# Performance work log

Measured on AMD Instinct MI355X. Metric: run time of the kernel, lower is better.

## Reference

```python
import jax, jax.numpy as jnp
import numpy as np

EPS = 1e-06


def setup_inputs() -> dict:
    key = jax.random.key(0)
    k1, k2 = jax.random.split(key)
    B, S, D = 8, 4096, 1024
    embeddings = jax.random.normal(k1, (B, S, D), dtype=jnp.float32)
    curvature = jax.random.normal(k2, (B, S, D), dtype=jnp.float32)
    gamma = jnp.ones((D,), dtype=jnp.float32)
    beta = jnp.zeros((D,), dtype=jnp.float32)
    curvature_scale = jnp.full((1,), 0.1, dtype=jnp.float32)
    return {
        "embeddings": embeddings,
        "curvature": curvature,
        "gamma": gamma,
        "beta": beta,
        "curvature_scale": curvature_scale,
    }


def reference(embeddings, curvature, gamma, beta, curvature_scale):
    # Field-aware normalization (FieldNormalization.call):
    # standard mean/var norm over features, scaled by local curvature magnitude.
    mean = jnp.mean(embeddings, axis=-1, keepdims=True)          # [B,S,1]
    var = jnp.var(embeddings, axis=-1, keepdims=True)            # [B,S,1]
    normalized = (embeddings - mean) / jnp.sqrt(var + EPS)       # [B,S,D]
    # curvature magnitude per token: sqrt(sum(c^2) + eps)
    curv_mag = jnp.sqrt(jnp.sum(curvature * curvature, axis=-1, keepdims=True) + EPS)
    curvature_factor = 1.0 / (1.0 + curvature_scale * curv_mag)  # [B,S,1]
    normalized = normalized * curvature_factor
    return normalized * gamma + beta
```

## Files before the change

kernel.cpp:

```cpp
#include <hip/hip_runtime.h>

#define D 1024
#define EPS 1e-6f

__global__ __launch_bounds__(256) void fieldnorm_kernel(
    const float* __restrict__ emb,
    const float* __restrict__ curv,
    const float* __restrict__ gamma,
    const float* __restrict__ beta,
    const float* __restrict__ cscale,
    float* __restrict__ out)
{
    const int row = blockIdx.x;
    const int tid = threadIdx.x;
    const long long base = (long long)row * D;

    const float4 x = reinterpret_cast<const float4*>(emb + base)[tid];
    const float4 c = reinterpret_cast<const float4*>(curv + base)[tid];

    float sx  = (x.x + x.y) + (x.z + x.w);
    float sx2 = (x.x * x.x + x.y * x.y) + (x.z * x.z + x.w * x.w);
    float sc2 = (c.x * c.x + c.y * c.y) + (c.z * c.z + c.w * c.w);

    #pragma unroll
    for (int off = 32; off > 0; off >>= 1) {
        sx  += __shfl_down(sx,  off, 64);
        sx2 += __shfl_down(sx2, off, 64);
        sc2 += __shfl_down(sc2, off, 64);
    }

    __shared__ float red[3][4];
    const int wave = tid >> 6;
    if ((tid & 63) == 0) {
        red[0][wave] = sx;
        red[1][wave] = sx2;
        red[2][wave] = sc2;
    }
    __syncthreads();
    sx  = (red[0][0] + red[0][1]) + (red[0][2] + red[0][3]);
    sx2 = (red[1][0] + red[1][1]) + (red[1][2] + red[1][3]);
    sc2 = (red[2][0] + red[2][1]) + (red[2][2] + red[2][3]);

    const float inv_d = 1.0f / (float)D;
    const float mean  = sx * inv_d;
    const float var   = sx2 * inv_d - mean * mean;
    const float rstd  = rsqrtf(var + EPS);
    const float cmag  = sqrtf(sc2 + EPS);
    const float fac   = 1.0f / (1.0f + cscale[0] * cmag);
    const float s     = rstd * fac;

    const float4 g = reinterpret_cast<const float4*>(gamma)[tid];
    const float4 b = reinterpret_cast<const float4*>(beta)[tid];

    float4 o;
    o.x = (x.x - mean) * s * g.x + b.x;
    o.y = (x.y - mean) * s * g.y + b.y;
    o.z = (x.z - mean) * s * g.z + b.z;
    o.w = (x.w - mean) * s * g.w + b.w;
    reinterpret_cast<float4*>(out + base)[tid] = o;
}

extern "C" void kernel_launch(void* const* d_in, const int* in_sizes, int n_in,
                              void* d_out, int out_size, void* d_ws, size_t ws_size,
                              hipStream_t stream) {
    const float* emb    = (const float*)d_in[0];
    const float* curv   = (const float*)d_in[1];
    const float* gamma  = (const float*)d_in[2];
    const float* beta   = (const float*)d_in[3];
    const float* cscale = (const float*)d_in[4];
    float* out = (float*)d_out;

    const int rows = out_size / D;
    fieldnorm_kernel<<<rows, 256, 0, stream>>>(emb, curv, gamma, beta, cscale, out);
}
```

Measured before the change: 72.52 us.

## Assign one row per wavefront and use nontemporal output stores

After: 60.75 us. 1.19x faster.

```diff
diff --git a/kernel.cpp b/kernel.cpp
--- a/kernel.cpp
+++ b/kernel.cpp
@@ -2,6 +2,8 @@
 
 #define D 1024
 #define EPS 1e-6f
+
+typedef float floatx4 __attribute__((ext_vector_type(4)));
 
 __global__ __launch_bounds__(256) void fieldnorm_kernel(
     const float* __restrict__ emb,
@@ -11,35 +13,39 @@
     const float* __restrict__ cscale,
     float* __restrict__ out)
 {
-    const int row = blockIdx.x;
-    const int tid = threadIdx.x;
+    const int wave = threadIdx.x >> 6;
+    const int lane = threadIdx.x & 63;
+    const int row  = blockIdx.x * 4 + wave;
     const long long base = (long long)row * D;
 
-    const float4 x = reinterpret_cast<const float4*>(emb + base)[tid];
-    const float4 c = reinterpret_cast<const float4*>(curv + base)[tid];
+    const floatx4* __restrict__ xp = reinterpret_cast<const floatx4*>(emb + base);
+    const floatx4* __restrict__ cp = reinterpret_cast<const floatx4*>(curv + base);
 
-    float sx  = (x.x + x.y) + (x.z + x.w);
-    float sx2 = (x.x * x.x + x.y * x.y) + (x.z * x.z + x.w * x.w);
-    float sc2 = (c.x * c.x + c.y * c.y) + (c.z * c.z + c.w * c.w);
+    floatx4 x[4];
+    #pragma unroll
+    for (int j = 0; j < 4; ++j) x[j] = xp[lane + 64 * j];
+
+    float sc2 = 0.0f;
+    #pragma unroll
+    for (int j = 0; j < 4; ++j) {
+        const floatx4 c = cp[lane + 64 * j];
+        sc2 += (c.x * c.x + c.y * c.y) + (c.z * c.z + c.w * c.w);
+    }
+
+    float sx = 0.0f, sx2 = 0.0f;
+    #pragma unroll
+    for (int j = 0; j < 4; ++j) {
+        sx  += (x[j].x + x[j].y) + (x[j].z + x[j].w);
+        sx2 += (x[j].x * x[j].x + x[j].y * x[j].y)
+             + (x[j].z * x[j].z + x[j].w * x[j].w);
+    }
 
     #pragma unroll
     for (int off = 32; off > 0; off >>= 1) {
-        sx  += __shfl_down(sx,  off, 64);
-        sx2 += __shfl_down(sx2, off, 64);
-        sc2 += __shfl_down(sc2, off, 64);
+        sx  += __shfl_xor(sx,  off, 64);
+        sx2 += __shfl_xor(sx2, off, 64);
+        sc2 += __shfl_xor(sc2, off, 64);
     }
-
-    __shared__ float red[3][4];
-    const int wave = tid >> 6;
-    if ((tid & 63) == 0) {
-        red[0][wave] = sx;
-        red[1][wave] = sx2;
-        red[2][wave] = sc2;
-    }
-    __syncthreads();
-    sx  = (red[0][0] + red[0][1]) + (red[0][2] + red[0][3]);
-    sx2 = (red[1][0] + red[1][1]) + (red[1][2] + red[1][3]);
-    sc2 = (red[2][0] + red[2][1]) + (red[2][2] + red[2][3]);
 
     const float inv_d = 1.0f / (float)D;
     const float mean  = sx * inv_d;
@@ -49,15 +55,22 @@
     const float fac   = 1.0f / (1.0f + cscale[0] * cmag);
     const float s     = rstd * fac;
 
-    const float4 g = reinterpret_cast<const float4*>(gamma)[tid];
-    const float4 b = reinterpret_cast<const float4*>(beta)[tid];
+    const floatx4* __restrict__ gp = reinterpret_cast<const floatx4*>(gamma);
+    const floatx4* __restrict__ bp = reinterpret_cast<const floatx4*>(beta);
+    floatx4* __restrict__ op = reinterpret_cast<floatx4*>(out + base);
 
-    float4 o;
-    o.x = (x.x - mean) * s * g.x + b.x;
-    o.y = (x.y - mean) * s * g.y + b.y;
-    o.z = (x.z - mean) * s * g.z + b.z;
-    o.w = (x.w - mean) * s * g.w + b.w;
-    reinterpret_cast<float4*>(out + base)[tid] = o;
+    #pragma unroll
+    for (int j = 0; j < 4; ++j) {
+        const int idx = lane + 64 * j;
+        const floatx4 g = gp[idx];
+        const floatx4 b = bp[idx];
+        floatx4 o;
+        o.x = (x[j].x - mean) * s * g.x + b.x;
+        o.y = (x[j].y - mean) * s * g.y + b.y;
+        o.z = (x[j].z - mean) * s * g.z + b.z;
+        o.w = (x[j].w - mean) * s * g.w + b.w;
+        __builtin_nontemporal_store(o, &op[idx]);
+    }
 }
 
 extern "C" void kernel_launch(void* const* d_in, const int* in_sizes, int n_in,
@@ -71,5 +84,5 @@
     float* out = (float*)d_out;
 
     const int rows = out_size / D;
-    fieldnorm_kernel<<<rows, 256, 0, stream>>>(emb, curv, gamma, beta, cscale, out);
+    fieldnorm_kernel<<<rows / 4, 256, 0, stream>>>(emb, curv, gamma, beta, cscale, out);
 }
```

## Process rows per wavefront with double-buffered loads and nontemporal accesses

Applied to the files above, without the earlier changes.

Result: faster. 63.54 us (-12.4%).

```diff
diff --git a/kernel.cpp b/kernel.cpp
--- a/kernel.cpp
+++ b/kernel.cpp
@@ -2,6 +2,8 @@
 
 #define D 1024
 #define EPS 1e-6f
+
+typedef float f4 __attribute__((ext_vector_type(4)));
 
 __global__ __launch_bounds__(256) void fieldnorm_kernel(
     const float* __restrict__ emb,
@@ -11,53 +13,81 @@
     const float* __restrict__ cscale,
     float* __restrict__ out)
 {
-    const int row = blockIdx.x;
-    const int tid = threadIdx.x;
-    const long long base = (long long)row * D;
+    const int wave = threadIdx.x >> 6;
+    const int lane = threadIdx.x & 63;
+    const int wid  = blockIdx.x * 4 + wave;
+    const int NW   = gridDim.x * 4;
 
-    const float4 x = reinterpret_cast<const float4*>(emb + base)[tid];
-    const float4 c = reinterpret_cast<const float4*>(curv + base)[tid];
+    f4 g[4], b[4];
+    #pragma unroll
+    for (int j = 0; j < 4; ++j) {
+        g[j] = reinterpret_cast<const f4*>(gamma)[lane + 64 * j];
+        b[j] = reinterpret_cast<const f4*>(beta)[lane + 64 * j];
+    }
+    const float cs    = cscale[0];
+    const float inv_d = 1.0f / (float)D;
 
-    float sx  = (x.x + x.y) + (x.z + x.w);
-    float sx2 = (x.x * x.x + x.y * x.y) + (x.z * x.z + x.w * x.w);
-    float sc2 = (c.x * c.x + c.y * c.y) + (c.z * c.z + c.w * c.w);
+    const long long base0 = (long long)(wid + 0 * NW) * D;
+    const long long base1 = (long long)(wid + 1 * NW) * D;
+    const long long base2 = (long long)(wid + 2 * NW) * D;
+    const long long base3 = (long long)(wid + 3 * NW) * D;
 
-    #pragma unroll
-    for (int off = 32; off > 0; off >>= 1) {
-        sx  += __shfl_down(sx,  off, 64);
-        sx2 += __shfl_down(sx2, off, 64);
-        sc2 += __shfl_down(sc2, off, 64);
-    }
+    f4 xa[4], ca[4], xb[4], cb[4];
 
-    __shared__ float red[3][4];
-    const int wave = tid >> 6;
-    if ((tid & 63) == 0) {
-        red[0][wave] = sx;
-        red[1][wave] = sx2;
-        red[2][wave] = sc2;
-    }
-    __syncthreads();
-    sx  = (red[0][0] + red[0][1]) + (red[0][2] + red[0][3]);
-    sx2 = (red[1][0] + red[1][1]) + (red[1][2] + red[1][3]);
-    sc2 = (red[2][0] + red[2][1]) + (red[2][2] + red[2][3]);
+#define LOADROW(X, C, BASE)                                                   \
+    do {                                                                      \
+        const f4* __restrict__ xp = reinterpret_cast<const f4*>(emb + (BASE));\
+        const f4* __restrict__ cp = reinterpret_cast<const f4*>(curv + (BASE));\
+        _Pragma("unroll")                                                     \
+        for (int j = 0; j < 4; ++j) {                                         \
+            X[j] = xp[lane + 64 * j];                                         \
+            C[j] = __builtin_nontemporal_load(&cp[lane + 64 * j]);            \
+        }                                                                     \
+    } while (0)
 
-    const float inv_d = 1.0f / (float)D;
-    const float mean  = sx * inv_d;
-    const float var   = sx2 * inv_d - mean * mean;
-    const float rstd  = rsqrtf(var + EPS);
-    const float cmag  = sqrtf(sc2 + EPS);
-    const float fac   = 1.0f / (1.0f + cscale[0] * cmag);
-    const float s     = rstd * fac;
+#define PROCROW(X, C, BASE)                                                   \
+    do {                                                                      \
+        float sx = 0.f, sq = 0.f, sc = 0.f;                                   \
+        _Pragma("unroll")                                                     \
+        for (int j = 0; j < 4; ++j) {                                         \
+            sx += (X[j].x + X[j].y) + (X[j].z + X[j].w);                      \
+            sq += (X[j].x * X[j].x + X[j].y * X[j].y)                         \
+                + (X[j].z * X[j].z + X[j].w * X[j].w);                        \
+            sc += (C[j].x * C[j].x + C[j].y * C[j].y)                         \
+                + (C[j].z * C[j].z + C[j].w * C[j].w);                        \
+        }                                                                     \
+        _Pragma("unroll")                                                     \
+        for (int off = 32; off > 0; off >>= 1) {                              \
+            sx += __shfl_xor(sx, off, 64);                                    \
+            sq += __shfl_xor(sq, off, 64);                                    \
+            sc += __shfl_xor(sc, off, 64);                                    \
+        }                                                                     \
+        const float mean = sx * inv_d;                                        \
+        const float var  = sq * inv_d - mean * mean;                          \
+        const float s    = rsqrtf(var + EPS) / (1.0f + cs * sqrtf(sc + EPS));  \
+        f4* __restrict__ op = reinterpret_cast<f4*>(out + (BASE));            \
+        _Pragma("unroll")                                                     \
+        for (int j = 0; j < 4; ++j) {                                         \
+            f4 o;                                                             \
+            o.x = (X[j].x - mean) * s * g[j].x + b[j].x;                      \
+            o.y = (X[j].y - mean) * s * g[j].y + b[j].y;                      \
+            o.z = (X[j].z - mean) * s * g[j].z + b[j].z;                      \
+            o.w = (X[j].w - mean) * s * g[j].w + b[j].w;                      \
+            __builtin_nontemporal_store(o, &op[lane + 64 * j]);               \
+        }                                                                     \
+    } while (0)
 
-    const float4 g = reinterpret_cast<const float4*>(gamma)[tid];
-    const float4 b = reinterpret_cast<const float4*>(beta)[tid];
+    LOADROW(xa, ca, base0);
+    LOADROW(xb, cb, base1);
+    PROCROW(xa, ca, base0);
+    LOADROW(xa, ca, base2);
+    PROCROW(xb, cb, base1);
+    LOADROW(xb, cb, base3);
+    PROCROW(xa, ca, base2);
+    PROCROW(xb, cb, base3);
 
-    float4 o;
-    o.x = (x.x - mean) * s * g.x + b.x;
-    o.y = (x.y - mean) * s * g.y + b.y;
-    o.z = (x.z - mean) * s * g.z + b.z;
-    o.w = (x.w - mean) * s * g.w + b.w;
-    reinterpret_cast<float4*>(out + base)[tid] = o;
+#undef LOADROW
+#undef PROCROW
 }
 
 extern "C" void kernel_launch(void* const* d_in, const int* in_sizes, int n_in,
@@ -70,6 +100,8 @@
     const float* cscale = (const float*)d_in[4];
     float* out = (float*)d_out;
 
-    const int rows = out_size / D;
-    fieldnorm_kernel<<<rows, 256, 0, stream>>>(emb, curv, gamma, beta, cscale, out);
+    const int rows   = out_size / D;
+    const int waves  = rows / 4;
+    const int blocks = waves / 4;
+    fieldnorm_kernel<<<blocks, 256, 0, stream>>>(emb, curv, gamma, beta, cscale, out);
 }
```
